# Performance work log

Hardware: AMD Instinct MI355X
Metric: run time of the kernel (lower is better)

Reference implementation:

```python
import jax, jax.numpy as jnp
import numpy as np

HEADS = 16
DIM_HEAD = 64
SCALE = DIM_HEAD ** -0.5


def setup_inputs() -> dict:
    key = jax.random.key(0)
    k1, k2, k3, k4 = jax.random.split(key, 4)
    b, n, dim = 4, 4096, 1024
    dim_inner = HEADS * DIM_HEAD
    x = jax.random.normal(k1, (b, n, dim), dtype=jnp.float32)
    W_qkv = jax.random.normal(k2, (dim, dim_inner * 3), dtype=jnp.float32) * 0.02
    agent_tokens = jax.random.normal(k3, (HEADS, 128, DIM_HEAD), dtype=jnp.float32) * 0.02
    W_out = jax.random.normal(k4, (dim_inner, dim), dtype=jnp.float32) * 0.02
    return {"x": x, "W_qkv": W_qkv, "agent_tokens": agent_tokens, "W_out": W_out}


def reference(x, W_qkv, agent_tokens, W_out):
    b, n, _ = x.shape
    h, m, d = agent_tokens.shape
    # qkv projection: b n (3 h d) -> 3, b, h, n, d
    qkv = (x @ W_qkv).reshape(b, n, 3, h, d).transpose(2, 0, 3, 1, 4)
    q, k, v = qkv[0], qkv[1], qkv[2]
    a = agent_tokens * SCALE  # h m d, broadcast over batch
    qa_sim = jnp.einsum('bhid,hjd->bhij', q, a)   # b h n m
    ak_sim = jnp.einsum('hid,bhjd->bhij', a, k)   # b h m n
    qa_attn = jax.nn.softmax(qa_sim, axis=-1)
    ak_attn = jax.nn.softmax(ak_sim, axis=-1)
    out = jnp.einsum('bhij,bhjd->bhid', ak_attn, v)    # b h m d
    out = jnp.einsum('bhij,bhjd->bhid', qa_attn, out)  # b h n d
    out = out.transpose(0, 2, 1, 3).reshape(b, n, h * d)
    return out @ W_out
```

## Files before the change

kernel.cpp:

```cpp
#include <hip/hip_runtime.h>

typedef __bf16 bf16x8 __attribute__((ext_vector_type(8)));
typedef float f32x4 __attribute__((ext_vector_type(4)));
typedef unsigned short ushort8 __attribute__((ext_vector_type(8)));
typedef unsigned short u16;

#define MFMA16(a, b, c) __builtin_amdgcn_mfma_f32_16x16x32_bf16(a, b, c, 0, 0, 0)
#define FENCE() __builtin_amdgcn_sched_barrier(0)
#define BARRIER() do { FENCE(); __builtin_amdgcn_s_barrier(); FENCE(); } while (0)
#define VMCNT(n) do { asm volatile("s_waitcnt vmcnt(" #n ")"); FENCE(); } while (0)

__device__ __forceinline__ u16 f2bf(float v) {
  unsigned int u = __builtin_bit_cast(unsigned int, v);
  u += 0x7fffu + ((u >> 16) & 1u);
  return (u16)(u >> 16);
}

__device__ __forceinline__ void gload16(const u16* g, u16* l) {
  __builtin_amdgcn_global_load_lds((__attribute__((address_space(1))) void*)(g),
                                   (__attribute__((address_space(3))) void*)(l), 16, 0, 0);
}


__global__ __launch_bounds__(256) void conv_x_kernel(const float* __restrict__ in, u16* __restrict__ out) {
  size_t i = (size_t)blockIdx.x * 256 + threadIdx.x;
  const float4* p = (const float4*)in + i * 2;
  float4 a = p[0], b = p[1];
  ushort8 o;
  o[0] = f2bf(a.x); o[1] = f2bf(a.y); o[2] = f2bf(a.z); o[3] = f2bf(a.w);
  o[4] = f2bf(b.x); o[5] = f2bf(b.y); o[6] = f2bf(b.z); o[7] = f2bf(b.w);
  *((ushort8*)out + i) = o;
}

__global__ __launch_bounds__(256) void conv_wT_tiled(const float* __restrict__ W, u16* __restrict__ WT,
                                                     int K, int N) {
  __shared__ float tile[64][65];
  int nt = N >> 6;
  int kt = blockIdx.x / nt, nti = blockIdx.x - kt * nt;
  int k0 = kt << 6, n0 = nti << 6;
  int t = threadIdx.x;
  int r = t >> 4, c4 = (t & 15) << 2;
#pragma unroll
  for (int j = 0; j < 4; ++j) {
    float4 v = *(const float4*)&W[(size_t)(k0 + j * 16 + r) * N + n0 + c4];
    tile[j * 16 + r][c4] = v.x; tile[j * 16 + r][c4 + 1] = v.y;
    tile[j * 16 + r][c4 + 2] = v.z; tile[j * 16 + r][c4 + 3] = v.w;
  }
  __syncthreads();
  int rn = t >> 2, cs = (t & 3) << 4;
  ushort8 o0, o1;
#pragma unroll
  for (int e = 0; e < 8; ++e) { o0[e] = f2bf(tile[cs + e][rn]); o1[e] = f2bf(tile[cs + 8 + e][rn]); }
  u16* dst = WT + (size_t)(n0 + rn) * K + k0 + cs;
  *(ushort8*)dst = o0;
  *(ushort8*)(dst + 8) = o1;
}

__global__ __launch_bounds__(256) void conv_a_kernel(const float* __restrict__ in, u16* __restrict__ out) {
  int i = blockIdx.x * 256 + threadIdx.x;
  out[i] = f2bf(in[i] * 0.125f);
}

template <int MODE>
__global__ __launch_bounds__(512, 2) void gemm256(const u16* __restrict__ A, const u16* __restrict__ BT,
                                                  int M, int N, int K,
                                                  u16* __restrict__ qb, u16* __restrict__ kb,
                                                  u16* __restrict__ vb, float* __restrict__ outf) {
  extern __shared__ char smem[];
  const int NT = K >> 5;
  int ntiles = N >> 8;
  int nwg = (M >> 8) * ntiles;
  int bid = blockIdx.x;
  int wg = (bid & 7) * (nwg >> 3) + (bid >> 3);
  int tm = wg / ntiles, tn = wg - tm * ntiles;
  int rb = tm << 8, cb = tn << 8;
  int t = threadIdx.x;
  int w = t >> 6, lane = t & 63, li = lane & 15, lg = lane >> 4;
  int wr = w >> 2, wc = w & 3;

  const u16* srcA[2];
  const u16* srcB[2];
#pragma unroll
  for (int j = 0; j < 2; ++j) {
    int D = j * 8192 + t * 16;
    int L = D ^ (((D >> 7) & 3) << 4);
    int row = L >> 6, inb = L & 63;
    srcA[j] = A + (size_t)(rb + row) * K + (inb >> 1);
    srcB[j] = BT + (size_t)(cb + row) * K + (inb >> 1);
  }
#define STAGE_A(slot, kt) do { \
    gload16(srcA[0] + (kt) * 32, (u16*)(smem + (slot) * 32768 + t * 16)); \
    gload16(srcA[1] + (kt) * 32, (u16*)(smem + (slot) * 32768 + 8192 + t * 16)); } while (0)
#define STAGE_B(slot, kt) do { \
    gload16(srcB[0] + (kt) * 32, (u16*)(smem + (slot) * 32768 + 16384 + t * 16)); \
    gload16(srcB[1] + (kt) * 32, (u16*)(smem + (slot) * 32768 + 24576 + t * 16)); } while (0)

  int offA[8], offB[4];
#pragma unroll
  for (int m8 = 0; m8 < 8; ++m8) {
    int row = wr * 128 + m8 * 16 + li;
    int L = row * 64 + lg * 16;
    offA[m8] = L ^ (((L >> 7) & 3) << 4);
  }
#pragma unroll
  for (int n = 0; n < 4; ++n) {
    int row = wc * 64 + n * 16 + li;
    int L = row * 64 + lg * 16;
    offB[n] = 16384 + (L ^ (((L >> 7) & 3) << 4));
  }

  f32x4 acc[8][4];
#pragma unroll
  for (int m = 0; m < 8; ++m)
#pragma unroll
    for (int n = 0; n < 4; ++n) acc[m][n] = (f32x4){0.f, 0.f, 0.f, 0.f};

  bf16x8 aF[4], aS[4], b0[4], b1[4];

#define RD_A_LO(sb, d) do { d[0] = *(const bf16x8*)((sb) + offA[0]); d[1] = *(const bf16x8*)((sb) + offA[1]); \
                            d[2] = *(const bf16x8*)((sb) + offA[2]); d[3] = *(const bf16x8*)((sb) + offA[3]); } while (0)
#define RD_A_HI(sb, d) do { d[0] = *(const bf16x8*)((sb) + offA[4]); d[1] = *(const bf16x8*)((sb) + offA[5]); \
                            d[2] = *(const bf16x8*)((sb) + offA[6]); d[3] = *(const bf16x8*)((sb) + offA[7]); } while (0)
#define RD_B(sb, d)    do { d[0] = *(const bf16x8*)((sb) + offB[0]); d[1] = *(const bf16x8*)((sb) + offB[1]); \
                            d[2] = *(const bf16x8*)((sb) + offB[2]); d[3] = *(const bf16x8*)((sb) + offB[3]); } while (0)

#define PH_EVEN(t, BC, STG) do { \
    BARRIER(); \
    { char* sb_ = smem + ((t) & 3) * 32768; RD_A_HI(sb_, aS); } \
    if (STG) STAGE_A(((t) + 3) & 3, (t) + 3); \
    FENCE(); \
    __builtin_amdgcn_s_setprio(1); \
    _Pragma("unroll") for (int m = 0; m < 4; ++m) \
      _Pragma("unroll") for (int n = 0; n < 4; ++n) acc[m][n] = MFMA16(aF[m], BC[n], acc[m][n]); \
    __builtin_amdgcn_s_setprio(0); \
  } while (0)

#define PH_ODD(t, BC, BN, STG, RDNEXT, WAITOP) do { \
    WAITOP; \
    BARRIER(); \
    if (RDNEXT) { char* sb_ = smem + (((t) + 1) & 3) * 32768; RD_A_LO(sb_, aF); RD_B(sb_, BN); } \
    if (STG) STAGE_B(((t) + 3) & 3, (t) + 3); \
    FENCE(); \
    __builtin_amdgcn_s_setprio(1); \
    _Pragma("unroll") for (int m = 0; m < 4; ++m) \
      _Pragma("unroll") for (int n = 0; n < 4; ++n) acc[4 + m][n] = MFMA16(aS[m], BC[n], acc[4 + m][n]); \
    __builtin_amdgcn_s_setprio(0); \
  } while (0)

#define TILE(t, BC, BN, STG, RDNEXT, WAITOP) do { \
    PH_EVEN(t, BC, STG); \
    PH_ODD(t, BC, BN, STG, RDNEXT, WAITOP); \
  } while (0)

  STAGE_A(0, 0); STAGE_B(0, 0);
  STAGE_A(1, 1); STAGE_B(1, 1);
  STAGE_A(2, 2); STAGE_B(2, 2);
  VMCNT(8);
  BARRIER();
  RD_A_LO(smem, aF); RD_B(smem, b0);

  for (int tt = 0; tt <= NT - 6; tt += 2) {
    TILE(tt,     b0, b1, 1, 1, VMCNT(6));
    TILE(tt + 1, b1, b0, 1, 1, VMCNT(6));
  }
  TILE(NT - 4, b0, b1, 1, 1, VMCNT(6));
  TILE(NT - 3, b1, b0, 0, 1, VMCNT(4));
  TILE(NT - 2, b0, b1, 0, 1, VMCNT(0));
  TILE(NT - 1, b1, b0, 0, 0, ((void)0));

  if (MODE == 0) {
    int col0 = cb + wc * 64;
    int s = col0 >> 10, hh = (col0 >> 6) & 15;
    u16* dst = (s == 0) ? qb : ((s == 1) ? kb : vb);
#pragma unroll
    for (int m = 0; m < 8; ++m) {
      int rbase = rb + wr * 128 + m * 16 + lg * 4;
#pragma unroll
      for (int r = 0; r < 4; ++r) {
        int rr = rbase + r;
        size_t o = (((size_t)(rr >> 12) * 16 + hh) * 4096 + (rr & 4095)) * 64;
#pragma unroll
        for (int n = 0; n < 4; ++n) dst[o + n * 16 + li] = f2bf(acc[m][n][r]);
      }
    }
  } else {
#pragma unroll
    for (int m = 0; m < 8; ++m) {
#pragma unroll
      for (int r = 0; r < 4; ++r) {
        float* po = outf + (size_t)(rb + wr * 128 + m * 16 + lg * 4 + r) * N + cb + wc * 64;
#pragma unroll
        for (int n = 0; n < 4; ++n) po[n * 16 + li] = acc[m][n][r];
      }
    }
  }
#undef TILE
#undef PH_ODD
#undef PH_EVEN
#undef RD_A_LO
#undef RD_A_HI
#undef RD_B
#undef STAGE_A
#undef STAGE_B
}

__global__ __launch_bounds__(256) void transpose_v(const u16* __restrict__ v, u16* __restrict__ vt) {
  __shared__ u16 tile[64][72];
  int bid = blockIdx.x;
  int bh = bid >> 6, n0 = (bid & 63) << 6;
  int t = threadIdx.x;
  int nl = t >> 2, ds = (t & 3) << 4;
  const u16* src = v + ((size_t)bh * 4096 + n0 + nl) * 64 + ds;
  *(uint4*)&tile[nl][ds] = *(const uint4*)src;
  *(uint4*)&tile[nl][ds + 8] = *(const uint4*)(src + 8);
  __syncthreads();
  int d = t >> 2, ns = (t & 3) << 4;
  ushort8 o0, o1;
#pragma unroll
  for (int e = 0; e < 8; ++e) { o0[e] = tile[ns + e][d]; o1[e] = tile[ns + 8 + e][d]; }
  u16* dst = vt + ((size_t)bh * 64 + d) * 4096 + n0 + ns;
  *(ushort8*)dst = o0;
  *(ushort8*)(dst + 8) = o1;
}

__global__ __launch_bounds__(256) void ak_flash(const u16* __restrict__ kb, const u16* __restrict__ vt,
                                                const u16* __restrict__ ab,
                                                float* __restrict__ pO, float* __restrict__ pM,
                                                float* __restrict__ pL) {
  __shared__ u16 p_lds[128][136];
  int bid = blockIdx.x;
  int s = bid & 7;
  int bh = bid >> 3;
  int h = bh & 15;
  int t = threadIdx.x, w = t >> 6, l = t & 63, lg = l >> 4, li = l & 15;
  int jb = w * 32;

  bf16x8 afr[2][2];
#pragma unroll
  for (int jt = 0; jt < 2; ++jt)
#pragma unroll
    for (int kk = 0; kk < 2; ++kk)
      afr[jt][kk] = *(const bf16x8*)&ab[(size_t)(h * 128 + jb + jt * 16 + li) * 64 + kk * 32 + lg * 8];

  f32x4 O[2][4];
  float mrow[2][4], lrow[2][4];
#pragma unroll
  for (int jt = 0; jt < 2; ++jt) {
#pragma unroll
    for (int dt = 0; dt < 4; ++dt) O[jt][dt] = (f32x4){0.f, 0.f, 0.f, 0.f};
#pragma unroll
    for (int r = 0; r < 4; ++r) { mrow[jt][r] = -1e30f; lrow[jt][r] = 0.f; }
  }
  const u16* kbase = kb + (size_t)bh * 4096 * 64;
  const u16* vbase = vt + (size_t)bh * 64 * 4096;

  for (int c = 0; c < 4; ++c) {
    int i0 = s * 512 + c * 128;
    f32x4 sf[2][8];
#pragma unroll
    for (int jt = 0; jt < 2; ++jt)
#pragma unroll
      for (int it = 0; it < 8; ++it) sf[jt][it] = (f32x4){0.f, 0.f, 0.f, 0.f};
#pragma unroll
    for (int it = 0; it < 8; ++it)
#pragma unroll
      for (int kk = 0; kk < 2; ++kk) {
        bf16x8 bfr = *(const bf16x8*)&kbase[(size_t)(i0 + it * 16 + li) * 64 + kk * 32 + lg * 8];
        sf[0][it] = MFMA16(afr[0][kk], bfr, sf[0][it]);
        sf[1][it] = MFMA16(afr[1][kk], bfr, sf[1][it]);
      }
#pragma unroll
    for (int jt = 0; jt < 2; ++jt)
#pragma unroll
      for (int r = 0; r < 4; ++r) {
        float cm = sf[jt][0][r];
#pragma unroll
        for (int it = 1; it < 8; ++it) cm = fmaxf(cm, sf[jt][it][r]);
#pragma unroll
        for (int off = 1; off < 16; off <<= 1) cm = fmaxf(cm, __shfl_xor(cm, off));
        float mold = mrow[jt][r];
        float mnew = fmaxf(mold, cm);
        float scale = __expf(mold - mnew);
        float ss = 0.f;
#pragma unroll
        for (int it = 0; it < 8; ++it) {
          float p = __expf(sf[jt][it][r] - mnew);
          sf[jt][it][r] = p;
          ss += p;
        }
#pragma unroll
        for (int off = 1; off < 16; off <<= 1) ss += __shfl_xor(ss, off);
        lrow[jt][r] = lrow[jt][r] * scale + ss;
        mrow[jt][r] = mnew;
#pragma unroll
        for (int dt = 0; dt < 4; ++dt) O[jt][dt][r] *= scale;
      }
#pragma unroll
    for (int jt = 0; jt < 2; ++jt)
#pragma unroll
      for (int it = 0; it < 8; ++it)
#pragma unroll
        for (int r = 0; r < 4; ++r)
          p_lds[jb + jt * 16 + lg * 4 + r][it * 16 + li] = f2bf(sf[jt][it][r]);
#pragma unroll
    for (int ks = 0; ks < 4; ++ks) {
      bf16x8 pa0 = *(const bf16x8*)&p_lds[jb + li][ks * 32 + lg * 8];
      bf16x8 pa1 = *(const bf16x8*)&p_lds[jb + 16 + li][ks * 32 + lg * 8];
#pragma unroll
      for (int dt = 0; dt < 4; ++dt) {
        bf16x8 bv = *(const bf16x8*)&vbase[(size_t)(dt * 16 + li) * 4096 + i0 + ks * 32 + lg * 8];
        O[0][dt] = MFMA16(pa0, bv, O[0][dt]);
        O[1][dt] = MFMA16(pa1, bv, O[1][dt]);
      }
    }
  }
  size_t pb = ((size_t)bh * 8 + s) * 128;
#pragma unroll
  for (int jt = 0; jt < 2; ++jt)
#pragma unroll
    for (int dt = 0; dt < 4; ++dt)
#pragma unroll
      for (int r = 0; r < 4; ++r) {
        int j = jb + jt * 16 + lg * 4 + r;
        pO[(pb + j) * 64 + dt * 16 + li] = O[jt][dt][r];
      }
  if (li == 0) {
#pragma unroll
    for (int jt = 0; jt < 2; ++jt)
#pragma unroll
      for (int r = 0; r < 4; ++r) {
        int j = jb + jt * 16 + lg * 4 + r;
        pM[pb + j] = mrow[jt][r];
        pL[pb + j] = lrow[jt][r];
      }
  }
}

__global__ __launch_bounds__(128) void ak_combine(const float* __restrict__ pO, const float* __restrict__ pM,
                                                  const float* __restrict__ pL, u16* __restrict__ out1t) {
  int bh = blockIdx.x;
  int j = threadIdx.x;
  float ms[8], wv[8];
  float M = -1e30f;
#pragma unroll
  for (int s = 0; s < 8; ++s) { ms[s] = pM[((size_t)bh * 8 + s) * 128 + j]; M = fmaxf(M, ms[s]); }
  float L = 0.f;
#pragma unroll
  for (int s = 0; s < 8; ++s) { wv[s] = __expf(ms[s] - M); L += wv[s] * pL[((size_t)bh * 8 + s) * 128 + j]; }
  float inv = 1.f / L;
  for (int d = 0; d < 64; ++d) {
    float acc = 0.f;
#pragma unroll
    for (int s = 0; s < 8; ++s) acc += wv[s] * pO[(((size_t)bh * 8 + s) * 128 + j) * 64 + d];
    out1t[((size_t)bh * 64 + d) * 128 + j] = f2bf(acc * inv);
  }
}

__global__ __launch_bounds__(256) void qa_fused(const u16* __restrict__ qb, const u16* __restrict__ out1t,
                                                const u16* __restrict__ ab, u16* __restrict__ out2) {
  __shared__ u16 p_lds[128][136];
  int bid = blockIdx.x;
  int nt = bid & 31;
  int bh = bid >> 5;
  int h = bh & 15, b = bh >> 4;
  int t = threadIdx.x, w = t >> 6, l = t & 63, lg = l >> 4, li = l & 15;
  int n0 = nt * 128;

  const u16* qbase = qb + ((size_t)bh * 4096 + n0 + w * 32) * 64;
  bf16x8 qf[2][2];
#pragma unroll
  for (int rt = 0; rt < 2; ++rt)
#pragma unroll
    for (int kk = 0; kk < 2; ++kk)
      qf[rt][kk] = *(const bf16x8*)&qbase[(size_t)(rt * 16 + li) * 64 + kk * 32 + lg * 8];

  f32x4 sf[2][8];
#pragma unroll
  for (int rt = 0; rt < 2; ++rt)
#pragma unroll
    for (int jt = 0; jt < 8; ++jt) sf[rt][jt] = (f32x4){0.f, 0.f, 0.f, 0.f};

  const u16* abase = ab + h * 128 * 64;
#pragma unroll
  for (int jt = 0; jt < 8; ++jt)
#pragma unroll
    for (int kk = 0; kk < 2; ++kk) {
      bf16x8 bfr = *(const bf16x8*)&abase[(size_t)(jt * 16 + li) * 64 + kk * 32 + lg * 8];
      sf[0][jt] = MFMA16(qf[0][kk], bfr, sf[0][jt]);
      sf[1][jt] = MFMA16(qf[1][kk], bfr, sf[1][jt]);
    }
  float inv[2][4];
#pragma unroll
  for (int rt = 0; rt < 2; ++rt)
#pragma unroll
    for (int r = 0; r < 4; ++r) {
      float cm = sf[rt][0][r];
#pragma unroll
      for (int jt = 1; jt < 8; ++jt) cm = fmaxf(cm, sf[rt][jt][r]);
#pragma unroll
      for (int off = 1; off < 16; off <<= 1) cm = fmaxf(cm, __shfl_xor(cm, off));
      float ss = 0.f;
#pragma unroll
      for (int jt = 0; jt < 8; ++jt) {
        float p = __expf(sf[rt][jt][r] - cm);
        sf[rt][jt][r] = p;
        ss += p;
      }
#pragma unroll
      for (int off = 1; off < 16; off <<= 1) ss += __shfl_xor(ss, off);
      inv[rt][r] = 1.f / ss;
    }
#pragma unroll
  for (int rt = 0; rt < 2; ++rt)
#pragma unroll
    for (int jt = 0; jt < 8; ++jt)
#pragma unroll
      for (int r = 0; r < 4; ++r)
        p_lds[w * 32 + rt * 16 + lg * 4 + r][jt * 16 + li] = f2bf(sf[rt][jt][r]);

  f32x4 O[2][4];
#pragma unroll
  for (int rt = 0; rt < 2; ++rt)
#pragma unroll
    for (int dt = 0; dt < 4; ++dt) O[rt][dt] = (f32x4){0.f, 0.f, 0.f, 0.f};

  const u16* obase = out1t + (size_t)bh * 64 * 128;
#pragma unroll
  for (int ks = 0; ks < 4; ++ks) {
    bf16x8 pa0 = *(const bf16x8*)&p_lds[w * 32 + li][ks * 32 + lg * 8];
    bf16x8 pa1 = *(const bf16x8*)&p_lds[w * 32 + 16 + li][ks * 32 + lg * 8];
#pragma unroll
    for (int dt = 0; dt < 4; ++dt) {
      bf16x8 bv = *(const bf16x8*)&obase[(size_t)(dt * 16 + li) * 128 + ks * 32 + lg * 8];
      O[0][dt] = MFMA16(pa0, bv, O[0][dt]);
      O[1][dt] = MFMA16(pa1, bv, O[1][dt]);
    }
  }
#pragma unroll
  for (int rt = 0; rt < 2; ++rt)
#pragma unroll
    for (int dt = 0; dt < 4; ++dt)
#pragma unroll
      for (int r = 0; r < 4; ++r) {
        int nn = n0 + w * 32 + rt * 16 + lg * 4 + r;
        int col = h * 64 + dt * 16 + li;
        out2[((size_t)b * 4096 + nn) * 1024 + col] = f2bf(O[rt][dt][r] * inv[rt][r]);
      }
}

extern "C" void kernel_launch(void* const* d_in, const int* in_sizes, int n_in,
                              void* d_out, int out_size, void* d_ws, size_t ws_size,
                              hipStream_t stream) {
  const float* x = (const float*)d_in[0];
  const float* Wqkv = (const float*)d_in[1];
  const float* agent = (const float*)d_in[2];
  const float* Wout = (const float*)d_in[3];
  float* out = (float*)d_out;

  char* ws = (char*)d_ws;
  u16* x_bf  = (u16*)(ws + 0);
  u16* wqkvT = (u16*)(ws + 33554432);
  u16* woutT = (u16*)(ws + 39845888);
  u16* a_bf  = (u16*)(ws + 41943040);
  u16* qb    = (u16*)(ws + 42205184);
  u16* kb    = (u16*)(ws + 75759616);
  u16* vb    = (u16*)(ws + 109314048);
  u16* vt    = (u16*)(ws + 142868480);
  float* pO  = (float*)(ws + 176422912);
  float* pM  = (float*)(ws + 193200128);
  float* pL  = (float*)(ws + 193724416);
  u16* out1t = (u16*)(ws + 194248704);
  u16* out2  = x_bf;

  (void)hipFuncSetAttribute((const void*)gemm256<0>, hipFuncAttributeMaxDynamicSharedMemorySize, 131072);
  (void)hipFuncSetAttribute((const void*)gemm256<1>, hipFuncAttributeMaxDynamicSharedMemorySize, 131072);

  conv_x_kernel<<<8192, 256, 0, stream>>>(x, x_bf);
  conv_wT_tiled<<<768, 256, 0, stream>>>(Wqkv, wqkvT, 1024, 3072);
  conv_wT_tiled<<<256, 256, 0, stream>>>(Wout, woutT, 1024, 1024);
  conv_a_kernel<<<512, 256, 0, stream>>>(agent, a_bf);

  gemm256<0><<<768, 512, 131072, stream>>>(x_bf, wqkvT, 16384, 3072, 1024, qb, kb, vb, nullptr);
  transpose_v<<<4096, 256, 0, stream>>>(vb, vt);
  ak_flash<<<512, 256, 0, stream>>>(kb, vt, a_bf, pO, pM, pL);
  ak_combine<<<64, 128, 0, stream>>>(pO, pM, pL, out1t);
  qa_fused<<<2048, 256, 0, stream>>>(qb, out1t, a_bf, out2);
  gemm256<1><<<256, 512, 131072, stream>>>(out2, woutT, 16384, 1024, 1024, nullptr, nullptr, nullptr, out);
}
```

Measured before the change: 300.5 us.

## Merge prep conversions into one kernel and write V transposed from QKV GEMM

Combines the four fp32-to-bf16 conversion kernels into a single launch that dispatches on block index. The QKV GEMM epilogue now writes the V slice directly in transposed (d-major) layout, so the separate transpose_v kernel and the intermediate V buffer are removed. This saves launches and a full read/write pass over V. The trade-off is that the transposed epilogue stores are strided by 4096 elements per lane, which is poorly coalesced.

```diff
diff --git a/kernel.cpp b/kernel.cpp
--- a/kernel.cpp
+++ b/kernel.cpp
@@ -21,24 +21,34 @@
                                    (__attribute__((address_space(3))) void*)(l), 16, 0, 0);
 }
 
-
-__global__ __launch_bounds__(256) void conv_x_kernel(const float* __restrict__ in, u16* __restrict__ out) {
-  size_t i = (size_t)blockIdx.x * 256 + threadIdx.x;
-  const float4* p = (const float4*)in + i * 2;
-  float4 a = p[0], b = p[1];
-  ushort8 o;
-  o[0] = f2bf(a.x); o[1] = f2bf(a.y); o[2] = f2bf(a.z); o[3] = f2bf(a.w);
-  o[4] = f2bf(b.x); o[5] = f2bf(b.y); o[6] = f2bf(b.z); o[7] = f2bf(b.w);
-  *((ushort8*)out + i) = o;
-}
-
-__global__ __launch_bounds__(256) void conv_wT_tiled(const float* __restrict__ W, u16* __restrict__ WT,
-                                                     int K, int N) {
+__global__ __launch_bounds__(256) void prep(const float* __restrict__ x, u16* __restrict__ x_bf,
+                                            const float* __restrict__ Wqkv, u16* __restrict__ wqkvT,
+                                            const float* __restrict__ Wout, u16* __restrict__ woutT,
+                                            const float* __restrict__ agent, u16* __restrict__ a_bf) {
   __shared__ float tile[64][65];
+  int bid = blockIdx.x;
+  int t = threadIdx.x;
+  if (bid < 8192) {
+    size_t i = (size_t)bid * 256 + t;
+    const float4* p = (const float4*)x + i * 2;
+    float4 a = p[0], b = p[1];
+    ushort8 o;
+    o[0] = f2bf(a.x); o[1] = f2bf(a.y); o[2] = f2bf(a.z); o[3] = f2bf(a.w);
+    o[4] = f2bf(b.x); o[5] = f2bf(b.y); o[6] = f2bf(b.z); o[7] = f2bf(b.w);
+    *((ushort8*)x_bf + i) = o;
+    return;
+  }
+  if (bid >= 9216) {
+    int i = (bid - 9216) * 256 + t;
+    a_bf[i] = f2bf(agent[i] * 0.125f);
+    return;
+  }
+  const float* W; u16* WT; int K = 1024, N; int b2;
+  if (bid < 8960) { W = Wqkv; WT = wqkvT; N = 3072; b2 = bid - 8192; }
+  else            { W = Wout; WT = woutT; N = 1024; b2 = bid - 8960; }
   int nt = N >> 6;
-  int kt = blockIdx.x / nt, nti = blockIdx.x - kt * nt;
+  int kt = b2 / nt, nti = b2 - kt * nt;
   int k0 = kt << 6, n0 = nti << 6;
-  int t = threadIdx.x;
   int r = t >> 4, c4 = (t & 15) << 2;
 #pragma unroll
   for (int j = 0; j < 4; ++j) {
@@ -56,16 +66,11 @@
   *(ushort8*)(dst + 8) = o1;
 }
 
-__global__ __launch_bounds__(256) void conv_a_kernel(const float* __restrict__ in, u16* __restrict__ out) {
-  int i = blockIdx.x * 256 + threadIdx.x;
-  out[i] = f2bf(in[i] * 0.125f);
-}
-
 template <int MODE>
 __global__ __launch_bounds__(512, 2) void gemm256(const u16* __restrict__ A, const u16* __restrict__ BT,
                                                   int M, int N, int K,
                                                   u16* __restrict__ qb, u16* __restrict__ kb,
-                                                  u16* __restrict__ vb, float* __restrict__ outf) {
+                                                  u16* __restrict__ vt, float* __restrict__ outf) {
   extern __shared__ char smem[];
   const int NT = K >> 5;
   int ntiles = N >> 8;
@@ -171,16 +176,32 @@
   if (MODE == 0) {
     int col0 = cb + wc * 64;
     int s = col0 >> 10, hh = (col0 >> 6) & 15;
-    u16* dst = (s == 0) ? qb : ((s == 1) ? kb : vb);
-#pragma unroll
-    for (int m = 0; m < 8; ++m) {
-      int rbase = rb + wr * 128 + m * 16 + lg * 4;
-#pragma unroll
-      for (int r = 0; r < 4; ++r) {
-        int rr = rbase + r;
-        size_t o = (((size_t)(rr >> 12) * 16 + hh) * 4096 + (rr & 4095)) * 64;
-#pragma unroll
-        for (int n = 0; n < 4; ++n) dst[o + n * 16 + li] = f2bf(acc[m][n][r]);
+    if (s < 2) {
+      u16* dst = (s == 0) ? qb : kb;
+#pragma unroll
+      for (int m = 0; m < 8; ++m) {
+        int rbase = rb + wr * 128 + m * 16 + lg * 4;
+#pragma unroll
+        for (int r = 0; r < 4; ++r) {
+          int rr = rbase + r;
+          size_t o = (((size_t)(rr >> 12) * 16 + hh) * 4096 + (rr & 4095)) * 64;
+#pragma unroll
+          for (int n = 0; n < 4; ++n) dst[o + n * 16 + li] = f2bf(acc[m][n][r]);
+        }
+      }
+    } else {
+#pragma unroll
+      for (int m = 0; m < 8; ++m) {
+        int rbase = rb + wr * 128 + m * 16 + lg * 4;
+#pragma unroll
+        for (int r = 0; r < 4; ++r) {
+          int rr = rbase + r;
+          size_t bh64 = ((size_t)(rr >> 12) * 16 + hh) * 64;
+          int nn = rr & 4095;
+#pragma unroll
+          for (int n = 0; n < 4; ++n)
+            vt[(bh64 + n * 16 + li) * 4096 + nn] = f2bf(acc[m][n][r]);
+        }
       }
     }
   } else {
@@ -202,25 +223,6 @@
 #undef RD_B
 #undef STAGE_A
 #undef STAGE_B
-}
-
-__global__ __launch_bounds__(256) void transpose_v(const u16* __restrict__ v, u16* __restrict__ vt) {
-  __shared__ u16 tile[64][72];
-  int bid = blockIdx.x;
-  int bh = bid >> 6, n0 = (bid & 63) << 6;
-  int t = threadIdx.x;
-  int nl = t >> 2, ds = (t & 3) << 4;
-  const u16* src = v + ((size_t)bh * 4096 + n0 + nl) * 64 + ds;
-  *(uint4*)&tile[nl][ds] = *(const uint4*)src;
-  *(uint4*)&tile[nl][ds + 8] = *(const uint4*)(src + 8);
-  __syncthreads();
-  int d = t >> 2, ns = (t & 3) << 4;
-  ushort8 o0, o1;
-#pragma unroll
-  for (int e = 0; e < 8; ++e) { o0[e] = tile[ns + e][d]; o1[e] = tile[ns + 8 + e][d]; }
-  u16* dst = vt + ((size_t)bh * 64 + d) * 4096 + n0 + ns;
-  *(ushort8*)dst = o0;
-  *(ushort8*)(dst + 8) = o1;
 }
 
 __global__ __launch_bounds__(256) void ak_flash(const u16* __restrict__ kb, const u16* __restrict__ vt,
@@ -464,7 +466,6 @@
   u16* a_bf  = (u16*)(ws + 41943040);
   u16* qb    = (u16*)(ws + 42205184);
   u16* kb    = (u16*)(ws + 75759616);
-  u16* vb    = (u16*)(ws + 109314048);
   u16* vt    = (u16*)(ws + 142868480);
   float* pO  = (float*)(ws + 176422912);
   float* pM  = (float*)(ws + 193200128);
@@ -475,13 +476,8 @@
   (void)hipFuncSetAttribute((const void*)gemm256<0>, hipFuncAttributeMaxDynamicSharedMemorySize, 131072);
   (void)hipFuncSetAttribute((const void*)gemm256<1>, hipFuncAttributeMaxDynamicSharedMemorySize, 131072);
 
-  conv_x_kernel<<<8192, 256, 0, stream>>>(x, x_bf);
-  conv_wT_tiled<<<768, 256, 0, stream>>>(Wqkv, wqkvT, 1024, 3072);
-  conv_wT_tiled<<<256, 256, 0, stream>>>(Wout, woutT, 1024, 1024);
-  conv_a_kernel<<<512, 256, 0, stream>>>(agent, a_bf);
-
-  gemm256<0><<<768, 512, 131072, stream>>>(x_bf, wqkvT, 16384, 3072, 1024, qb, kb, vb, nullptr);
-  transpose_v<<<4096, 256, 0, stream>>>(vb, vt);
+  prep<<<9728, 256, 0, stream>>>(x, x_bf, Wqkv, wqkvT, Wout, woutT, agent, a_bf);
+  gemm256<0><<<768, 512, 131072, stream>>>(x_bf, wqkvT, 16384, 3072, 1024, qb, kb, vt, nullptr);
   ak_flash<<<512, 256, 0, stream>>>(kb, vt, a_bf, pO, pM, pL);
   ak_combine<<<64, 128, 0, stream>>>(pO, pM, pL, out1t);
   qa_fused<<<2048, 256, 0, stream>>>(qb, out1t, a_bf, out2);
```

Result: faster. 285.0 us (-5.2%).
